# Kernel optimization log

Measured on AMD Instinct MI355X. Metric: run time of the kernel, lower is better.

The kernel has to match this reference:

```python
import jax, jax.numpy as jnp
import numpy as np

B, C, N = 8, 128, 4096  # (batch, channels=dim, time); F = N//2+1 = 2049 (odd)


def setup_inputs() -> dict:
    key = jax.random.key(0)
    ks = jax.random.split(key, 7)
    s = 1.0 / np.sqrt(C)
    return {
        "x_in": jax.random.normal(ks[0], (B, C, N), dtype=jnp.float32),
        "W_K": jax.random.normal(ks[1], (C, C), dtype=jnp.float32) * s,
        "b_K": jax.random.normal(ks[2], (C,), dtype=jnp.float32) * s,
        "W_V": jax.random.normal(ks[3], (C, C), dtype=jnp.float32) * s,
        "b_V": jax.random.normal(ks[4], (C,), dtype=jnp.float32) * s,
        "w_high": jax.random.normal(ks[5], (C, 2), dtype=jnp.float32) * 0.02,
        "threshold_param": jax.random.uniform(ks[6], (1,), dtype=jnp.float32) * 0.5,
    }


def reference(x_in, W_K, b_K, W_V, b_V, w_high, threshold_param):
    x = jnp.transpose(x_in, (0, 2, 1)).astype(jnp.float32)  # (B, N, C)
    _, n, c = x.shape
    x_fft = jnp.fft.rfft(x, axis=1, norm="ortho")            # (B, F, C) complex64
    K = jnp.fft.rfft(x @ W_K.T + b_K, axis=1, norm="ortho")  # (B, F, C)
    V = jnp.fft.rfft(x @ W_V.T + b_V, axis=1, norm="ortho")  # (B, F, C)
    scale = c ** (-0.5)
    # complex attention scores (no conjugation, matching torch.matmul(Q, K^T))
    attn = jnp.einsum("bfc,bgc->bfg", x_fft, K) * scale      # (B, F, F) complex
    attn = jax.nn.softmax(jnp.abs(attn), axis=-1)            # real softmax of |scores|
    context = jnp.einsum("bfg,bgc->bfc", attn.astype(x_fft.dtype), V)
    # adaptive high-frequency mask
    energy = jnp.sum(jnp.abs(x_fft) ** 2, axis=-1)           # (B, F)
    median_energy = jnp.median(energy, axis=1, keepdims=True)
    normalized = energy / (median_energy + 1e-6)
    threshold = jnp.quantile(normalized, threshold_param[0])  # global quantile
    mask = (normalized > threshold)[:, :, None]               # (B, F, 1)
    w_hi = w_high[:, 0] + 1j * w_high[:, 1]                   # (C,) complex
    context = context + jnp.where(mask, x_fft, 0.0) * w_hi
    out = jnp.fft.irfft(context, n=n, axis=1, norm="ortho")  # (B, N, C) float32
    return jnp.transpose(out, (0, 2, 1))                      # (B, C, N)
```

## Files before the change

### kernel.cpp

```cpp
#include <hip/hip_runtime.h>
#include <math.h>

#define NB 8
#define NC 128
#define NT 4096
#define NF 2049
#define FP 2176

typedef __bf16 bf16;
typedef __bf16 bf16x2 __attribute__((ext_vector_type(2)));
typedef __bf16 bf16x8 __attribute__((ext_vector_type(8)));
typedef float f32x4 __attribute__((ext_vector_type(4)));
typedef unsigned int uint32x4 __attribute__((ext_vector_type(4)));

__device__ __forceinline__ void async16(const bf16* g, bf16* l) {
    __builtin_amdgcn_global_load_lds(
        (const __attribute__((address_space(1))) void*)g,
        (__attribute__((address_space(3))) void*)l, 16, 0, 0);
}

__device__ __forceinline__ bf16x8 derive_b2(bf16x8 v) {
    uint32x4 u = __builtin_bit_cast(uint32x4, v);
#pragma unroll
    for (int i = 0; i < 4; ++i)
        u[i] = (((u[i] >> 16) | (u[i] << 16)) ^ 0x00008000u);
    return __builtin_bit_cast(bf16x8, u);
}

__device__ __forceinline__ float2 cmulf(float2 a, float2 b) {
    return make_float2(a.x * b.x - a.y * b.y, a.x * b.y + a.y * b.x);
}

__global__ __launch_bounds__(256) void prep_kernel(const float* __restrict__ W_K,
                                                   const float* __restrict__ W_V,
                                                   float2* __restrict__ tw,
                                                   bf16* __restrict__ Wk1,
                                                   bf16* __restrict__ Av) {
    int idx = blockIdx.x * 256 + threadIdx.x;
    if (idx < 2048) {
        float ang = (float)M_PI * (float)idx * (1.0f / 2048.0f);
        float sw, cw;
        __sincosf(ang, &sw, &cw);
        tw[idx] = make_float2(cw, -sw);
    }
    int n = idx >> 8, k = idx & 255;
    int c = k >> 1;
    int j = n >> 1;
    float v = 0.f;
    if (!(n & 1) && !(k & 1)) v = W_K[j * NC + c];
    else if ((n & 1) && (k & 1)) v = -W_K[j * NC + c];
    Wk1[idx] = (bf16)v;
    float v2 = 0.f;
    if (!(n & 1) && !(k & 1)) v2 = W_V[j * NC + c];
    else if ((n & 1) && (k & 1)) v2 = W_V[j * NC + c];
    Av[idx] = (bf16)v2;
}

__device__ __forceinline__ void fft4096(float2* buf, const float2* __restrict__ tw) {
    int sh = 0;
#pragma unroll
    for (int s6 = 0; s6 < 6; ++s6) {
        int L = 1 << sh;
        __syncthreads();
        for (int t = threadIdx.x; t < 1024; t += 256) {
            int pos = t & (L - 1);
            int base = ((t >> sh) << (sh + 2)) + pos;
            int k1 = pos << (10 - sh);
            float2 w1 = tw[k1];
            float2 w2 = tw[2 * k1];
            float2 w3 = cmulf(w1, w2);
            float2 x0 = buf[base];
            float2 x1 = cmulf(buf[base + L], w1);
            float2 x2 = cmulf(buf[base + 2 * L], w2);
            float2 x3 = cmulf(buf[base + 3 * L], w3);
            float2 b0 = make_float2(x0.x + x2.x, x0.y + x2.y);
            float2 b1 = make_float2(x0.x - x2.x, x0.y - x2.y);
            float2 b2 = make_float2(x1.x + x3.x, x1.y + x3.y);
            float2 b3 = make_float2(x1.x - x3.x, x1.y - x3.y);
            buf[base]         = make_float2(b0.x + b2.x, b0.y + b2.y);
            buf[base + L]     = make_float2(b1.x + b3.y, b1.y - b3.x);
            buf[base + 2 * L] = make_float2(b0.x - b2.x, b0.y - b2.y);
            buf[base + 3 * L] = make_float2(b1.x - b3.y, b1.y + b3.x);
        }
        sh += 2;
    }
    __syncthreads();
}

__device__ __forceinline__ unsigned dr4(unsigned i) {
    unsigned r = __brev(i) >> 20;
    return ((r & 0x555u) << 1) | ((r & 0xAAAu) >> 1);
}

__global__ __launch_bounds__(256) void fft_fwd_kernel(const float* __restrict__ x_in,
                                                      const float2* __restrict__ tw,
                                                      float2* __restrict__ Xc) {
    __shared__ float2 buf[NT];
    int bc = blockIdx.x;
    const float* xrow = x_in + (size_t)bc * NT;
    for (int i = threadIdx.x; i < NT; i += 256)
        buf[dr4((unsigned)i)] = make_float2(xrow[i], 0.0f);
    fft4096(buf, tw);
    const float inv = 1.0f / 64.0f;
    float2* orow = Xc + (size_t)bc * NF;
    for (int f = threadIdx.x; f < NF; f += 256) {
        float2 v = buf[f];
        orow[f] = make_float2(v.x * inv, v.y * inv);
    }
}

__global__ __launch_bounds__(256) void xt_kernel(const float2* __restrict__ Xc,
                                                 float2* __restrict__ Xf2,
                                                 bf16* __restrict__ Xb,
                                                 float* __restrict__ Ep) {
    __shared__ float2 tile[64][65];
    int blk = blockIdx.x;
    int b = blk / 68;
    int t2 = blk % 68;
    int chalf = t2 / 34;
    int c0 = chalf * 64;
    int f0 = (t2 % 34) * 64;
    int t = threadIdx.x;
    int fl = t & 63, cc = t >> 6;
#pragma unroll
    for (int cb = 0; cb < 16; ++cb) {
        int cl = cb * 4 + cc;
        int f = f0 + fl;
        float2 v = make_float2(0.f, 0.f);
        if (f < NF) v = Xc[((size_t)b * NC + c0 + cl) * NF + f];
        tile[fl][cl] = v;
    }
    __syncthreads();
    int chl = t & 63, ww = t >> 6;
    float epart[16];
#pragma unroll
    for (int wb = 0; wb < 16; ++wb) {
        int fl2 = wb * 4 + ww;
        int f = f0 + fl2;
        float2 v = tile[fl2][chl];
        epart[wb] = v.x * v.x + v.y * v.y;
        if (f < NF) Xf2[((size_t)b * NF + f) * 128 + c0 + chl] = v;
        bf16x2 p;
        p[0] = (bf16)v.x; p[1] = (bf16)v.y;
        *(bf16x2*)&Xb[((size_t)b * FP + f) * 256 + 2 * (c0 + chl)] = p;
    }
    __syncthreads();
    float* es = (float*)tile;
#pragma unroll
    for (int wb = 0; wb < 16; ++wb)
        es[(wb * 4 + ww) * 65 + chl] = epart[wb];
    __syncthreads();
    if (t < 64 && f0 + t < NF) {
        float s = 0.f;
#pragma unroll
        for (int c = 0; c < 64; ++c) s += es[t * 65 + c];
        Ep[((size_t)b * 2 + chalf) * FP + f0 + t] = s;
    }
}

__device__ __forceinline__ void gemm_body(const bf16* Abase, const bf16* Bbase,
                                          bf16* As, bf16* Bs,
                                          f32x4 (&acc)[4][4],
                                          int wave, int lane) {
    int m = lane & 15, quad = lane >> 4;
    int row_off = (wave & 1) * 64, col_off = (wave >> 1) * 64;
    int lrow = lane >> 3;
    int cswz = (lane & 7) ^ lrow;
    int mk = m & 7;
    for (int kk = 0; kk < 256; kk += 64) {
        __syncthreads();
#pragma unroll
        for (int t = 0; t < 4; ++t) {
            int r0 = wave * 32 + t * 8;
            async16(Abase + (size_t)(r0 + lrow) * 256 + kk + cswz * 8, As + r0 * 64);
            async16(Bbase + (size_t)(r0 + lrow) * 256 + kk + cswz * 8, Bs + r0 * 64);
        }
        __syncthreads();
#pragma unroll
        for (int k2 = 0; k2 < 64; k2 += 32) {
            bf16x8 a[4], bb[4];
            int pos = (((k2 >> 3) + quad) ^ mk) << 3;
#pragma unroll
            for (int i = 0; i < 4; ++i) a[i] = *(const bf16x8*)&As[(row_off + i * 16 + m) * 64 + pos];
#pragma unroll
            for (int j = 0; j < 4; ++j) bb[j] = *(const bf16x8*)&Bs[(col_off + j * 16 + m) * 64 + pos];
#pragma unroll
            for (int i = 0; i < 4; ++i)
#pragma unroll
                for (int j = 0; j < 4; ++j)
                    acc[i][j] = __builtin_amdgcn_mfma_f32_16x16x32_bf16(a[i], bb[j], acc[i][j], 0, 0, 0);
        }
    }
}

__global__ __launch_bounds__(256, 2) void kvvt_kernel(const bf16* __restrict__ Xb,
                                                      const bf16* __restrict__ Wk1,
                                                      const bf16* __restrict__ Av,
                                                      const float* __restrict__ b_K,
                                                      const float* __restrict__ b_V,
                                                      bf16* __restrict__ K1,
                                                      bf16* __restrict__ Vt) {
    __shared__ __align__(16) bf16 As[128 * 64];
    __shared__ __align__(16) bf16 Bs[128 * 64];
    int blk = blockIdx.x;
    int tid = threadIdx.x;
    int wave = tid >> 6, lane = tid & 63;
    int m = lane & 15, quad = lane >> 4;
    int row_off = (wave & 1) * 64, col_off = (wave >> 1) * 64;
    f32x4 acc[4][4] = {};
    const int HALF = NB * 17 * 2;
    if (blk < HALF * 1) {
        int b = blk & 7;
        int t2 = blk >> 3;
        int g0 = (t2 >> 1) * 128;
        int n0 = (t2 & 1) * 128;
        gemm_body(Xb + ((size_t)b * FP + g0) * 256, Wk1 + (size_t)n0 * 256,
                  As, Bs, acc, wave, lane);
#pragma unroll
        for (int i = 0; i < 4; ++i)
#pragma unroll
            for (int j = 0; j < 4; ++j)
#pragma unroll
                for (int r = 0; r < 4; ++r) {
                    int row = g0 + row_off + i * 16 + quad * 4 + r;
                    int col = n0 + col_off + j * 16 + m;
                    float val = acc[i][j][r];
                    if (row == 0 && !(col & 1)) val += 64.0f * b_K[col >> 1];
                    K1[((size_t)b * FP + row) * 256 + col] = (bf16)val;
                }
    } else {
        int blk2 = blk - HALF;
        int b = blk2 & 7;
        int t2 = blk2 >> 3;
        int g0 = (t2 >> 1) * 128;
        int n0 = (t2 & 1) * 128;
        gemm_body(Av + (size_t)n0 * 256, Xb + ((size_t)b * FP + g0) * 256,
                  As, Bs, acc, wave, lane);
#pragma unroll
        for (int i = 0; i < 4; ++i)
#pragma unroll
            for (int j = 0; j < 4; ++j)
#pragma unroll
                for (int r = 0; r < 4; ++r) {
                    int row = n0 + row_off + i * 16 + quad * 4 + r;
                    int col = g0 + col_off + j * 16 + m;
                    float val = acc[i][j][r];
                    if (col == 0 && !(row & 1)) val += 64.0f * b_V[row >> 1];
                    Vt[((size_t)b * 256 + row) * FP + col] = (bf16)val;
                }
    }
}

__global__ __launch_bounds__(256) void median_kernel(const float* __restrict__ Ep,
                                                     float* __restrict__ med) {
    int blk = blockIdx.x;
    int b = blk / 9, chunk = blk % 9;
    __shared__ __align__(16) float e[2052];
    const float* e0 = Ep + (size_t)b * 2 * FP;
    const float* e1 = e0 + FP;
    for (int i = threadIdx.x; i < 2052; i += 256)
        e[i] = (i < NF) ? (e0[i] + e1[i]) : INFINITY;
    __syncthreads();
    int i = chunk * 256 + threadIdx.x;
    float ei = (i < NF) ? e[i] : 0.f;
    int rank = 0;
#pragma unroll 4
    for (int j4 = 0; j4 < 513; ++j4) {
        float4 v = ((const float4*)e)[j4];
        int j = j4 * 4;
        rank += (v.x < ei) || (v.x == ei && j + 0 < i);
        rank += (v.y < ei) || (v.y == ei && j + 1 < i);
        rank += (v.z < ei) || (v.z == ei && j + 2 < i);
        rank += (v.w < ei) || (v.w == ei && j + 3 < i);
    }
    if (i < NF && rank == 1024) med[b] = ei;
}

__global__ __launch_bounds__(256) void rankpart_kernel(const float* __restrict__ Ep,
                                                       const float* __restrict__ med,
                                                       float* __restrict__ nrm,
                                                       int* __restrict__ rankpart) {
    const int n = NB * NF;
    int cb = blockIdx.x / 17;
    int chunk = blockIdx.x % 17;
    __shared__ __align__(16) float cdata[1024];
    int base = chunk * 1024;
    for (int t = threadIdx.x; t < 1024; t += 256) {
        int idx = base + t;
        float v = INFINITY;
        if (idx < n) {
            int b = idx / NF, f = idx % NF;
            float e = Ep[((size_t)b * 2) * FP + f] + Ep[((size_t)b * 2 + 1) * FP + f];
            v = e / (med[b] + 1e-6f);
        }
        cdata[t] = v;
    }
    __syncthreads();
    int i = cb * 256 + threadIdx.x;
    if (i >= n) return;
    int bi = i / NF, fi = i % NF;
    float ei = (Ep[((size_t)bi * 2) * FP + fi] + Ep[((size_t)bi * 2 + 1) * FP + fi]) /
               (med[bi] + 1e-6f);
    if (chunk == 0) nrm[i] = ei;
    int rank = 0;
#pragma unroll 8
    for (int t4 = 0; t4 < 256; ++t4) {
        float4 v = ((const float4*)cdata)[t4];
        int j = base + t4 * 4;
        rank += (v.x < ei) || (v.x == ei && j + 0 < i);
        rank += (v.y < ei) || (v.y == ei && j + 1 < i);
        rank += (v.z < ei) || (v.z == ei && j + 2 < i);
        rank += (v.w < ei) || (v.w == ei && j + 3 < i);
    }
    rankpart[(size_t)i * 17 + chunk] = rank;
}

__global__ __launch_bounds__(256) void rankreduce_kernel(const int* __restrict__ rankpart,
                                                         const float* __restrict__ nrm,
                                                         const float* __restrict__ q,
                                                         float* __restrict__ vk) {
    const int n = NB * NF;
    int i = blockIdx.x * 256 + threadIdx.x;
    if (i >= n) return;
    int rank = 0;
    const int* rp = rankpart + (size_t)i * 17;
#pragma unroll
    for (int c = 0; c < 17; ++c) rank += rp[c];
    double pos = (double)q[0] * (double)(n - 1);
    int k0 = (int)floor(pos);
    int k1 = min(k0 + 1, n - 1);
    if (rank == k0) vk[0] = nrm[i];
    if (rank == k1) vk[1] = nrm[i];
}

__global__ __launch_bounds__(256, 4) void score_kernel(const bf16* __restrict__ Xb,
                                                       const bf16* __restrict__ K1,
                                                       bf16* __restrict__ S,
                                                       float* __restrict__ Mpart,
                                                       float* __restrict__ Lpart) {
    __shared__ __align__(16) char smem[24576];
    bf16* As  = (bf16*)smem;
    bf16* B1s = (bf16*)(smem + 16384);
    int blk = blockIdx.x;
    int b = blk & 7;
    int t2 = blk >> 3;
    int f0 = (t2 / 34) * 128;
    int gblk = t2 % 34;
    int g0 = gblk * 64;
    int tid = threadIdx.x;
    int wave = tid >> 6, lane = tid & 63;
    int m = lane & 15, quad = lane >> 4;
    int row_off = (wave & 1) * 64, col_off = (wave >> 1) * 32;

    f32x4 accRe[4][2] = {};
    f32x4 accIm[4][2] = {};
    const bf16* Abase = Xb + ((size_t)b * FP + f0) * 256;
    const bf16* Kbase = K1 + ((size_t)b * FP + g0) * 256;
    int lrow = lane >> 3;
    int cswz = (lane & 7) ^ lrow;
    int mk = m & 7;

    for (int kk = 0; kk < 256; kk += 64) {
        __syncthreads();
#pragma unroll
        for (int t = 0; t < 4; ++t) {
            int r0 = wave * 32 + t * 8;
            async16(Abase + (size_t)(r0 + lrow) * 256 + kk + cswz * 8, As + r0 * 64);
        }
#pragma unroll
        for (int t = 0; t < 2; ++t) {
            int r0 = wave * 16 + t * 8;
            async16(Kbase + (size_t)(r0 + lrow) * 256 + kk + cswz * 8, B1s + r0 * 64);
        }
        __syncthreads();
#pragma unroll
        for (int k2 = 0; k2 < 64; k2 += 32) {
            bf16x8 a[4], b1[2], b2[2];
            int pos = (((k2 >> 3) + quad) ^ mk) << 3;
#pragma unroll
            for (int i = 0; i < 4; ++i)
                a[i] = *(const bf16x8*)&As[(row_off + i * 16 + m) * 64 + pos];
#pragma unroll
            for (int j = 0; j < 2; ++j) {
                b1[j] = *(const bf16x8*)&B1s[(col_off + j * 16 + m) * 64 + pos];
                b2[j] = derive_b2(b1[j]);
            }
#pragma unroll
            for (int i = 0; i < 4; ++i)
#pragma unroll
                for (int j = 0; j < 2; ++j) {
                    accRe[i][j] = __builtin_amdgcn_mfma_f32_16x16x32_bf16(a[i], b1[j], accRe[i][j], 0, 0, 0);
                    accIm[i][j] = __builtin_amdgcn_mfma_f32_16x16x32_bf16(a[i], b2[j], accIm[i][j], 0, 0, 0);
                }
        }
    }
    const float SCALE = 0.08838834764831845f;
    __syncthreads();
    bf16 (*Cs)[76] = (bf16(*)[76])smem;
#pragma unroll
    for (int i = 0; i < 4; ++i)
#pragma unroll
        for (int j = 0; j < 2; ++j)
#pragma unroll
            for (int r = 0; r < 4; ++r) {
                float re = accRe[i][j][r], im = accIm[i][j][r];
                Cs[row_off + i * 16 + quad * 4 + r][col_off + j * 16 + m] =
                    (bf16)(sqrtf(re * re + im * im) * SCALE);
            }
    __syncthreads();
    float* mred = (float*)(smem + 19456);
    float* lred = (float*)(smem + 20480);
    bf16* Sb = S + (size_t)b * FP * FP;
    int row = tid >> 1, half = tid & 1;
    const bf16* src = &Cs[row][half * 32];
    bf16* dst = Sb + (size_t)(f0 + row) * FP + g0 + half * 32;
    int gbase = g0 + half * 32;
    float vf[32];
#pragma unroll
    for (int u = 0; u < 4; ++u) {
        bf16x8 v8 = *(const bf16x8*)&src[u * 8];
        *(bf16x8*)&dst[u * 8] = v8;
#pragma unroll
        for (int e = 0; e < 8; ++e) vf[u * 8 + e] = (float)v8[e];
    }
    if (gblk >= 32) {
#pragma unroll
        for (int k = 0; k < 32; ++k)
            if (gbase + k > 2048) vf[k] = -1e30f;
    }
    float lmax = -1e30f;
#pragma unroll
    for (int k = 0; k < 32; ++k) lmax = fmaxf(lmax, vf[k]);
    mred[tid] = lmax;
    __syncthreads();
    float rmax = fmaxf(mred[row * 2], mred[row * 2 + 1]);
    float lsum = 0.f;
#pragma unroll
    for (int k = 0; k < 32; ++k) lsum += __expf(vf[k] - rmax);
    lred[tid] = lsum;
    __syncthreads();
    if (half == 0) {
        size_t ro = ((size_t)b * FP + f0 + row) * 34 + gblk;
        Mpart[ro] = rmax;
        Lpart[ro] = lred[row * 2] + lred[row * 2 + 1];
    }
}

__global__ __launch_bounds__(256, 3) void context_kernel(const bf16* __restrict__ Sg,
                                                         const float* __restrict__ Mpart,
                                                         const float* __restrict__ Lpart,
                                                         const bf16* __restrict__ Vt,
                                                         const float2* __restrict__ Xf2,
                                                         const float* __restrict__ nrm,
                                                         const float* __restrict__ vk,
                                                         const float* __restrict__ q,
                                                         const float* __restrict__ w_high,
                                                         float* __restrict__ Ctxt) {
    __shared__ __align__(16) char smem[36864];
    bf16* Ps = (bf16*)smem;
    bf16* Vs = (bf16*)(smem + 4096);
    int blk = blockIdx.x;
    int b = blk & 7;
    int f0 = (blk >> 3) * 32;
    int tid = threadIdx.x;
    int wave = tid >> 6, lane = tid & 63;
    int m = lane & 15, quad = lane >> 4;
    int col_off = wave * 64;
    int lrow = lane >> 3;
    int cswz = (lane & 7) ^ lrow;
    int mk = m & 7;

    f32x4 acc[2][4] = {};
    int prow = wave * 8 + lrow;
    const bf16* Prow = Sg + ((size_t)b * FP + f0 + prow) * FP;
    float cst;
    {
        const float* mp = Mpart + ((size_t)b * FP + f0 + prow) * 34;
        const float* lp = Lpart + ((size_t)b * FP + f0 + prow) * 34;
        float M = -1e30f;
#pragma unroll
        for (int i = 0; i < 34; ++i) M = fmaxf(M, mp[i]);
        float L = 0.f;
#pragma unroll
        for (int i = 0; i < 34; ++i) L += lp[i] * __expf(mp[i] - M);
        cst = M + __logf(L);
    }
    float thrv;
    {
        const int n = NB * NF;
        double pos = (double)q[0] * (double)(n - 1);
        double k0 = floor(pos);
        double frac = pos - k0;
        thrv = (float)((double)vk[0] + ((double)vk[1] - (double)vk[0]) * frac);
    }
    const bf16* Vbase = Vt + (size_t)b * 256 * FP;

    for (int kk = 0; kk < FP; kk += 64) {
        __syncthreads();
#pragma unroll
        for (int t = 0; t < 8; ++t) {
            int r0 = wave * 64 + t * 8;
            async16(Vbase + (size_t)(r0 + lrow) * FP + kk + cswz * 8, Vs + r0 * 64);
        }
        {
            bf16x8 s8 = *(const bf16x8*)&Prow[kk + cswz * 8];
            bf16x8 p8;
#pragma unroll
            for (int e = 0; e < 8; ++e) p8[e] = (bf16)__expf((float)s8[e] - cst);
            *(bf16x8*)&Ps[prow * 64 + (lane & 7) * 8] = p8;
        }
        __syncthreads();
#pragma unroll
        for (int k2 = 0; k2 < 64; k2 += 32) {
            bf16x8 a[2], bb[4];
            int pos = (((k2 >> 3) + quad) ^ mk) << 3;
#pragma unroll
            for (int i = 0; i < 2; ++i) a[i] = *(const bf16x8*)&Ps[(i * 16 + m) * 64 + pos];
#pragma unroll
            for (int j = 0; j < 4; ++j) bb[j] = *(const bf16x8*)&Vs[(col_off + j * 16 + m) * 64 + pos];
#pragma unroll
            for (int i = 0; i < 2; ++i)
#pragma unroll
                for (int j = 0; j < 4; ++j)
                    acc[i][j] = __builtin_amdgcn_mfma_f32_16x16x32_bf16(a[i], bb[j], acc[i][j], 0, 0, 0);
        }
    }
#pragma unroll
    for (int i = 0; i < 2; ++i)
#pragma unroll
        for (int r = 0; r < 4; ++r) {
            int row = f0 + i * 16 + quad * 4 + r;
            if (row < NF && nrm[b * NF + row] > thrv) {
#pragma unroll
                for (int j = 0; j < 4; ++j) {
                    int col = col_off + j * 16 + m;
                    int c = col >> 1;
                    float2 x = Xf2[((size_t)b * NF + row) * 128 + c];
                    float wr = w_high[2 * c], wi = w_high[2 * c + 1];
                    acc[i][j][r] += (col & 1) ? (x.x * wi + x.y * wr)
                                              : (x.x * wr - x.y * wi);
                }
            }
        }
    __syncthreads();
    float (*Ts)[33] = (float(*)[33])smem;
#pragma unroll
    for (int i = 0; i < 2; ++i)
#pragma unroll
        for (int j = 0; j < 4; ++j)
#pragma unroll
            for (int r = 0; r < 4; ++r) {
                int fl = i * 16 + quad * 4 + r;
                int col = col_off + j * 16 + m;
                Ts[col][fl] = acc[i][j][r];
            }
    __syncthreads();
    int f = tid & 31;
    int ch0 = tid >> 5;
    if (f0 + f < NF) {
#pragma unroll
        for (int p = 0; p < 32; ++p) {
            int ch = ch0 + p * 8;
            Ctxt[((size_t)b * 256 + ch) * NF + f0 + f] = Ts[ch][f];
        }
    }
}

__global__ __launch_bounds__(256) void fft_inv_kernel(const float* __restrict__ Ctxt,
                                                      const float2* __restrict__ tw,
                                                      float* __restrict__ out) {
    __shared__ float2 buf[NT];
    int bc = blockIdx.x, b = bc >> 7, c = bc & 127;
    const float* base = Ctxt + ((size_t)b * 256 + 2 * c) * NF;
    const float* basei = base + NF;
    for (int f = threadIdx.x; f < NT; f += 256) {
        float re, im;
        if (f <= NT / 2) {
            re = base[f];
            im = -basei[f];
        } else {
            int g = NT - f;
            re = base[g];
            im = basei[g];
        }
        buf[dr4((unsigned)f)] = make_float2(re, im);
    }
    fft4096(buf, tw);
    float* orow = out + (size_t)bc * NT;
    const float inv = 1.0f / 64.0f;
    for (int n = threadIdx.x; n < NT; n += 256) orow[n] = buf[n].x * inv;
}

extern "C" void kernel_launch(void* const* d_in, const int* in_sizes, int n_in,
                              void* d_out, int out_size, void* d_ws, size_t ws_size,
                              hipStream_t stream) {
    const float* x_in = (const float*)d_in[0];
    const float* W_K = (const float*)d_in[1];
    const float* b_K = (const float*)d_in[2];
    const float* W_V = (const float*)d_in[3];
    const float* b_V = (const float*)d_in[4];
    const float* w_high = (const float*)d_in[5];
    const float* qpar = (const float*)d_in[6];
    float* out = (float*)d_out;

    char* w = (char*)d_ws;
    const size_t SPECB = (size_t)NB * NF * 256 * 4;
    float* Xf = (float*)w;            w += SPECB;
    float* Ep = (float*)w;            w += (size_t)NB * 2 * FP * 4;
    float* med = (float*)w;           w += 64;
    float* nrm = (float*)w;           w += (size_t)NB * NF * 4;
    float* vk = (float*)w;            w += 64;
    w = (char*)(((uintptr_t)w + 255) & ~(uintptr_t)255);
    float2* tw = (float2*)w;          w += (size_t)2048 * 8;
    int* rankpart = (int*)w;          w += (size_t)16640 * 17 * 4;
    w = (char*)(((uintptr_t)w + 255) & ~(uintptr_t)255);
    float* Mpart = (float*)w;         w += (size_t)NB * FP * 34 * 4;
    float* Lpart = (float*)w;         w += (size_t)NB * FP * 34 * 4;
    w = (char*)(((uintptr_t)w + 255) & ~(uintptr_t)255);
    bf16* S = (bf16*)w;               w += (size_t)NB * FP * FP * 2;
    bf16* Xb = (bf16*)w;              w += (size_t)NB * FP * 256 * 2;
    bf16* K1 = (bf16*)w;              w += (size_t)NB * FP * 256 * 2;
    bf16* Vt = (bf16*)w;              w += (size_t)NB * 256 * FP * 2;
    bf16* Wk1 = (bf16*)w;             w += (size_t)256 * 256 * 2;
    bf16* Av = (bf16*)w;              w += (size_t)256 * 256 * 2;
    float2* Xc = (float2*)S;
    float* Ctxt = (float*)Xb;

    prep_kernel<<<256, 256, 0, stream>>>(W_K, W_V, tw, Wk1, Av);
    fft_fwd_kernel<<<NB * NC, 256, 0, stream>>>(x_in, tw, Xc);
    xt_kernel<<<NB * 2 * 34, 256, 0, stream>>>(Xc, (float2*)Xf, Xb, Ep);
    kvvt_kernel<<<NB * 17 * 2 * 2, 256, 0, stream>>>(Xb, Wk1, Av, b_K, b_V, K1, Vt);
    median_kernel<<<NB * 9, 256, 0, stream>>>(Ep, med);
    rankpart_kernel<<<65 * 17, 256, 0, stream>>>(Ep, med, nrm, rankpart);
    rankreduce_kernel<<<65, 256, 0, stream>>>(rankpart, nrm, qpar, vk);
    score_kernel<<<NB * 17 * 34, 256, 0, stream>>>(Xb, K1, S, Mpart, Lpart);
    context_kernel<<<NB * 65, 256, 0, stream>>>(S, Mpart, Lpart, Vt, (const float2*)Xf,
                                                nrm, vk, qpar, w_high, Ctxt);
    fft_inv_kernel<<<NB * NC, 256, 0, stream>>>(Ctxt, tw, out);
}
```

Measured before the change: 356.9 us.

## Merge side kernels into GEMM launches and compute FFT twiddles in LDS

Cuts the launch count from ten to seven. Weight prep now runs as extra blocks of the forward FFT kernel, the median runs as extra blocks of the K/V GEMM kernel, and the rank partials run as extra blocks of the score kernel. The twiddle table is no longer precomputed in global memory: each FFT block computes it into LDS with sincos. This removes launch gaps and lets the small independent jobs overlap with the large GEMMs. The cost is 16 KB more LDS per FFT block, which can lower occupancy, plus redundant sincos work in every block.

```diff
diff --git a/kernel.cpp b/kernel.cpp
--- a/kernel.cpp
+++ b/kernel.cpp
@@ -31,32 +31,16 @@
     return make_float2(a.x * b.x - a.y * b.y, a.x * b.y + a.y * b.x);
 }
 
-__global__ __launch_bounds__(256) void prep_kernel(const float* __restrict__ W_K,
-                                                   const float* __restrict__ W_V,
-                                                   float2* __restrict__ tw,
-                                                   bf16* __restrict__ Wk1,
-                                                   bf16* __restrict__ Av) {
-    int idx = blockIdx.x * 256 + threadIdx.x;
-    if (idx < 2048) {
-        float ang = (float)M_PI * (float)idx * (1.0f / 2048.0f);
+__device__ __forceinline__ void fill_tw(float2* twl) {
+    for (int k = threadIdx.x; k < 2048; k += 256) {
+        float ang = (float)M_PI * (float)k * (1.0f / 2048.0f);
         float sw, cw;
         __sincosf(ang, &sw, &cw);
-        tw[idx] = make_float2(cw, -sw);
-    }
-    int n = idx >> 8, k = idx & 255;
-    int c = k >> 1;
-    int j = n >> 1;
-    float v = 0.f;
-    if (!(n & 1) && !(k & 1)) v = W_K[j * NC + c];
-    else if ((n & 1) && (k & 1)) v = -W_K[j * NC + c];
-    Wk1[idx] = (bf16)v;
-    float v2 = 0.f;
-    if (!(n & 1) && !(k & 1)) v2 = W_V[j * NC + c];
-    else if ((n & 1) && (k & 1)) v2 = W_V[j * NC + c];
-    Av[idx] = (bf16)v2;
-}
-
-__device__ __forceinline__ void fft4096(float2* buf, const float2* __restrict__ tw) {
+        twl[k] = make_float2(cw, -sw);
+    }
+}
+
+__device__ __forceinline__ void fft4096(float2* buf, const float2* twl) {
     int sh = 0;
 #pragma unroll
     for (int s6 = 0; s6 < 6; ++s6) {
@@ -66,8 +50,8 @@
             int pos = t & (L - 1);
             int base = ((t >> sh) << (sh + 2)) + pos;
             int k1 = pos << (10 - sh);
-            float2 w1 = tw[k1];
-            float2 w2 = tw[2 * k1];
+            float2 w1 = twl[k1];
+            float2 w2 = twl[2 * k1];
             float2 w3 = cmulf(w1, w2);
             float2 x0 = buf[base];
             float2 x1 = cmulf(buf[base + L], w1);
@@ -92,17 +76,37 @@
     return ((r & 0x555u) << 1) | ((r & 0xAAAu) >> 1);
 }
 
-__global__ __launch_bounds__(256) void fft_fwd_kernel(const float* __restrict__ x_in,
-                                                      const float2* __restrict__ tw,
-                                                      float2* __restrict__ Xc) {
+__global__ __launch_bounds__(256) void fftfwd_kernel(const float* __restrict__ x_in,
+                                                     const float* __restrict__ W_K,
+                                                     const float* __restrict__ W_V,
+                                                     float2* __restrict__ Xc,
+                                                     bf16* __restrict__ Wk1,
+                                                     bf16* __restrict__ Av) {
     __shared__ float2 buf[NT];
-    int bc = blockIdx.x;
-    const float* xrow = x_in + (size_t)bc * NT;
+    __shared__ float2 twl[2048];
+    int blk = blockIdx.x;
+    if (blk >= NB * NC) {
+        int idx = (blk - NB * NC) * 256 + threadIdx.x;
+        int n = idx >> 8, k = idx & 255;
+        int c = k >> 1;
+        int j = n >> 1;
+        float v = 0.f;
+        if (!(n & 1) && !(k & 1)) v = W_K[j * NC + c];
+        else if ((n & 1) && (k & 1)) v = -W_K[j * NC + c];
+        Wk1[idx] = (bf16)v;
+        float v2 = 0.f;
+        if (!(n & 1) && !(k & 1)) v2 = W_V[j * NC + c];
+        else if ((n & 1) && (k & 1)) v2 = W_V[j * NC + c];
+        Av[idx] = (bf16)v2;
+        return;
+    }
+    fill_tw(twl);
+    const float* xrow = x_in + (size_t)blk * NT;
     for (int i = threadIdx.x; i < NT; i += 256)
         buf[dr4((unsigned)i)] = make_float2(xrow[i], 0.0f);
-    fft4096(buf, tw);
+    fft4096(buf, twl);
     const float inv = 1.0f / 64.0f;
-    float2* orow = Xc + (size_t)bc * NF;
+    float2* orow = Xc + (size_t)blk * NF;
     for (int f = threadIdx.x; f < NF; f += 256) {
         float2 v = buf[f];
         orow[f] = make_float2(v.x * inv, v.y * inv);
@@ -193,23 +197,50 @@
     }
 }
 
-__global__ __launch_bounds__(256, 2) void kvvt_kernel(const bf16* __restrict__ Xb,
-                                                      const bf16* __restrict__ Wk1,
-                                                      const bf16* __restrict__ Av,
-                                                      const float* __restrict__ b_K,
-                                                      const float* __restrict__ b_V,
-                                                      bf16* __restrict__ K1,
-                                                      bf16* __restrict__ Vt) {
-    __shared__ __align__(16) bf16 As[128 * 64];
-    __shared__ __align__(16) bf16 Bs[128 * 64];
+__global__ __launch_bounds__(256, 2) void kvvt_med_kernel(const bf16* __restrict__ Xb,
+                                                          const bf16* __restrict__ Wk1,
+                                                          const bf16* __restrict__ Av,
+                                                          const float* __restrict__ b_K,
+                                                          const float* __restrict__ b_V,
+                                                          const float* __restrict__ Ep,
+                                                          bf16* __restrict__ K1,
+                                                          bf16* __restrict__ Vt,
+                                                          float* __restrict__ med) {
+    __shared__ __align__(16) char smem[32768];
+    bf16* As = (bf16*)smem;
+    bf16* Bs = (bf16*)(smem + 16384);
     int blk = blockIdx.x;
     int tid = threadIdx.x;
+    const int HALF = NB * 17 * 2;
+    if (blk >= 2 * HALF) {
+        int mb = blk - 2 * HALF;
+        int b = mb / 9, chunk = mb % 9;
+        float* e = (float*)smem;
+        const float* e0 = Ep + (size_t)b * 2 * FP;
+        const float* e1 = e0 + FP;
+        for (int i = tid; i < 2052; i += 256)
+            e[i] = (i < NF) ? (e0[i] + e1[i]) : INFINITY;
+        __syncthreads();
+        int i = chunk * 256 + tid;
+        float ei = (i < NF) ? e[i] : 0.f;
+        int rank = 0;
+#pragma unroll 4
+        for (int j4 = 0; j4 < 513; ++j4) {
+            float4 v = ((const float4*)e)[j4];
+            int j = j4 * 4;
+            rank += (v.x < ei) || (v.x == ei && j + 0 < i);
+            rank += (v.y < ei) || (v.y == ei && j + 1 < i);
+            rank += (v.z < ei) || (v.z == ei && j + 2 < i);
+            rank += (v.w < ei) || (v.w == ei && j + 3 < i);
+        }
+        if (i < NF && rank == 1024) med[b] = ei;
+        return;
+    }
     int wave = tid >> 6, lane = tid & 63;
     int m = lane & 15, quad = lane >> 4;
     int row_off = (wave & 1) * 64, col_off = (wave >> 1) * 64;
     f32x4 acc[4][4] = {};
-    const int HALF = NB * 17 * 2;
-    if (blk < HALF * 1) {
+    if (blk < HALF) {
         int b = blk & 7;
         int t2 = blk >> 3;
         int g0 = (t2 >> 1) * 128;
@@ -251,70 +282,6 @@
     }
 }
 
-__global__ __launch_bounds__(256) void median_kernel(const float* __restrict__ Ep,
-                                                     float* __restrict__ med) {
-    int blk = blockIdx.x;
-    int b = blk / 9, chunk = blk % 9;
-    __shared__ __align__(16) float e[2052];
-    const float* e0 = Ep + (size_t)b * 2 * FP;
-    const float* e1 = e0 + FP;
-    for (int i = threadIdx.x; i < 2052; i += 256)
-        e[i] = (i < NF) ? (e0[i] + e1[i]) : INFINITY;
-    __syncthreads();
-    int i = chunk * 256 + threadIdx.x;
-    float ei = (i < NF) ? e[i] : 0.f;
-    int rank = 0;
-#pragma unroll 4
-    for (int j4 = 0; j4 < 513; ++j4) {
-        float4 v = ((const float4*)e)[j4];
-        int j = j4 * 4;
-        rank += (v.x < ei) || (v.x == ei && j + 0 < i);
-        rank += (v.y < ei) || (v.y == ei && j + 1 < i);
-        rank += (v.z < ei) || (v.z == ei && j + 2 < i);
-        rank += (v.w < ei) || (v.w == ei && j + 3 < i);
-    }
-    if (i < NF && rank == 1024) med[b] = ei;
-}
-
-__global__ __launch_bounds__(256) void rankpart_kernel(const float* __restrict__ Ep,
-                                                       const float* __restrict__ med,
-                                                       float* __restrict__ nrm,
-                                                       int* __restrict__ rankpart) {
-    const int n = NB * NF;
-    int cb = blockIdx.x / 17;
-    int chunk = blockIdx.x % 17;
-    __shared__ __align__(16) float cdata[1024];
-    int base = chunk * 1024;
-    for (int t = threadIdx.x; t < 1024; t += 256) {
-        int idx = base + t;
-        float v = INFINITY;
-        if (idx < n) {
-            int b = idx / NF, f = idx % NF;
-            float e = Ep[((size_t)b * 2) * FP + f] + Ep[((size_t)b * 2 + 1) * FP + f];
-            v = e / (med[b] + 1e-6f);
-        }
-        cdata[t] = v;
-    }
-    __syncthreads();
-    int i = cb * 256 + threadIdx.x;
-    if (i >= n) return;
-    int bi = i / NF, fi = i % NF;
-    float ei = (Ep[((size_t)bi * 2) * FP + fi] + Ep[((size_t)bi * 2 + 1) * FP + fi]) /
-               (med[bi] + 1e-6f);
-    if (chunk == 0) nrm[i] = ei;
-    int rank = 0;
-#pragma unroll 8
-    for (int t4 = 0; t4 < 256; ++t4) {
-        float4 v = ((const float4*)cdata)[t4];
-        int j = base + t4 * 4;
-        rank += (v.x < ei) || (v.x == ei && j + 0 < i);
-        rank += (v.y < ei) || (v.y == ei && j + 1 < i);
-        rank += (v.z < ei) || (v.z == ei && j + 2 < i);
-        rank += (v.w < ei) || (v.w == ei && j + 3 < i);
-    }
-    rankpart[(size_t)i * 17 + chunk] = rank;
-}
-
 __global__ __launch_bounds__(256) void rankreduce_kernel(const int* __restrict__ rankpart,
                                                          const float* __restrict__ nrm,
                                                          const float* __restrict__ q,
@@ -333,21 +300,63 @@
     if (rank == k1) vk[1] = nrm[i];
 }
 
-__global__ __launch_bounds__(256, 4) void score_kernel(const bf16* __restrict__ Xb,
-                                                       const bf16* __restrict__ K1,
-                                                       bf16* __restrict__ S,
-                                                       float* __restrict__ Mpart,
-                                                       float* __restrict__ Lpart) {
+__global__ __launch_bounds__(256, 4) void score_rank_kernel(const bf16* __restrict__ Xb,
+                                                            const bf16* __restrict__ K1,
+                                                            const float* __restrict__ Ep,
+                                                            const float* __restrict__ med,
+                                                            bf16* __restrict__ S,
+                                                            float* __restrict__ Mpart,
+                                                            float* __restrict__ Lpart,
+                                                            float* __restrict__ nrm,
+                                                            int* __restrict__ rankpart) {
     __shared__ __align__(16) char smem[24576];
+    int blk = blockIdx.x;
+    int tid = threadIdx.x;
+    const int NSCORE = NB * 17 * 34;
+    if (blk >= NSCORE) {
+        const int n = NB * NF;
+        int rb = blk - NSCORE;
+        int cb = rb / 17;
+        int chunk = rb % 17;
+        float* cdata = (float*)smem;
+        int base = chunk * 1024;
+        for (int t = tid; t < 1024; t += 256) {
+            int idx = base + t;
+            float v = INFINITY;
+            if (idx < n) {
+                int b = idx / NF, f = idx % NF;
+                float e = Ep[((size_t)b * 2) * FP + f] + Ep[((size_t)b * 2 + 1) * FP + f];
+                v = e / (med[b] + 1e-6f);
+            }
+            cdata[t] = v;
+        }
+        __syncthreads();
+        int i = cb * 256 + tid;
+        if (i >= n) return;
+        int bi = i / NF, fi = i % NF;
+        float ei = (Ep[((size_t)bi * 2) * FP + fi] + Ep[((size_t)bi * 2 + 1) * FP + fi]) /
+                   (med[bi] + 1e-6f);
+        if (chunk == 0) nrm[i] = ei;
+        int rank = 0;
+#pragma unroll 8
+        for (int t4 = 0; t4 < 256; ++t4) {
+            float4 v = ((const float4*)cdata)[t4];
+            int j = base + t4 * 4;
+            rank += (v.x < ei) || (v.x == ei && j + 0 < i);
+            rank += (v.y < ei) || (v.y == ei && j + 1 < i);
+            rank += (v.z < ei) || (v.z == ei && j + 2 < i);
+            rank += (v.w < ei) || (v.w == ei && j + 3 < i);
+        }
+        rankpart[(size_t)i * 17 + chunk] = rank;
+        return;
+    }
     bf16* As  = (bf16*)smem;
     bf16* B1s = (bf16*)(smem + 16384);
-    int blk = blockIdx.x;
     int b = blk & 7;
     int t2 = blk >> 3;
     int f0 = (t2 / 34) * 128;
     int gblk = t2 % 34;
     int g0 = gblk * 64;
-    int tid = threadIdx.x;
     int wave = tid >> 6, lane = tid & 63;
     int m = lane & 15, quad = lane >> 4;
     int row_off = (wave & 1) * 64, col_off = (wave >> 1) * 32;
@@ -567,10 +576,11 @@
 }
 
 __global__ __launch_bounds__(256) void fft_inv_kernel(const float* __restrict__ Ctxt,
-                                                      const float2* __restrict__ tw,
                                                       float* __restrict__ out) {
     __shared__ float2 buf[NT];
+    __shared__ float2 twl[2048];
     int bc = blockIdx.x, b = bc >> 7, c = bc & 127;
+    fill_tw(twl);
     const float* base = Ctxt + ((size_t)b * 256 + 2 * c) * NF;
     const float* basei = base + NF;
     for (int f = threadIdx.x; f < NT; f += 256) {
@@ -585,7 +595,7 @@
         }
         buf[dr4((unsigned)f)] = make_float2(re, im);
     }
-    fft4096(buf, tw);
+    fft4096(buf, twl);
     float* orow = out + (size_t)bc * NT;
     const float inv = 1.0f / 64.0f;
     for (int n = threadIdx.x; n < NT; n += 256) orow[n] = buf[n].x * inv;
@@ -611,7 +621,6 @@
     float* nrm = (float*)w;           w += (size_t)NB * NF * 4;
     float* vk = (float*)w;            w += 64;
     w = (char*)(((uintptr_t)w + 255) & ~(uintptr_t)255);
-    float2* tw = (float2*)w;          w += (size_t)2048 * 8;
     int* rankpart = (int*)w;          w += (size_t)16640 * 17 * 4;
     w = (char*)(((uintptr_t)w + 255) & ~(uintptr_t)255);
     float* Mpart = (float*)w;         w += (size_t)NB * FP * 34 * 4;
@@ -626,15 +635,14 @@
     float2* Xc = (float2*)S;
     float* Ctxt = (float*)Xb;
 
-    prep_kernel<<<256, 256, 0, stream>>>(W_K, W_V, tw, Wk1, Av);
-    fft_fwd_kernel<<<NB * NC, 256, 0, stream>>>(x_in, tw, Xc);
+    fftfwd_kernel<<<NB * NC + 256, 256, 0, stream>>>(x_in, W_K, W_V, Xc, Wk1, Av);
     xt_kernel<<<NB * 2 * 34, 256, 0, stream>>>(Xc, (float2*)Xf, Xb, Ep);
-    kvvt_kernel<<<NB * 17 * 2 * 2, 256, 0, stream>>>(Xb, Wk1, Av, b_K, b_V, K1, Vt);
-    median_kernel<<<NB * 9, 256, 0, stream>>>(Ep, med);
-    rankpart_kernel<<<65 * 17, 256, 0, stream>>>(Ep, med, nrm, rankpart);
+    kvvt_med_kernel<<<NB * 17 * 2 * 2 + NB * 9, 256, 0, stream>>>(
+        Xb, Wk1, Av, b_K, b_V, Ep, K1, Vt, med);
+    score_rank_kernel<<<NB * 17 * 34 + 65 * 17, 256, 0, stream>>>(
+        Xb, K1, Ep, med, S, Mpart, Lpart, nrm, rankpart);
     rankreduce_kernel<<<65, 256, 0, stream>>>(rankpart, nrm, qpar, vk);
-    score_kernel<<<NB * 17 * 34, 256, 0, stream>>>(Xb, K1, S, Mpart, Lpart);
     context_kernel<<<NB * 65, 256, 0, stream>>>(S, Mpart, Lpart, Vt, (const float2*)Xf,
                                                 nrm, vk, qpar, w_high, Ctxt);
-    fft_inv_kernel<<<NB * NC, 256, 0, stream>>>(Ctxt, tw, out);
-}
+    fft_inv_kernel<<<NB * NC, 256, 0, stream>>>(Ctxt, out);
+}
```

New measurement: 389.5 us. 1.09x slower.
